# Performance work log

Hardware: AMD Instinct MI355X
Metric: run time of the kernel (lower is better)

The kernel has to match this reference:

```python
import jax, jax.numpy as jnp
import numpy as np

N = 131072   # num_nodes
E = 262144   # events in the batch
D = 128      # memory_dim
R = 128      # raw_msg_dim
T = 32       # time_dim


def setup_inputs() -> dict:
    key = jax.random.key(0)
    ks = jax.random.split(key, 16)
    s = 0.05
    return {
        "memory": jax.random.normal(ks[0], (N, D), jnp.float32) * s,
        "raw_msg": jax.random.normal(ks[1], (E, R), jnp.float32) * s,
        "time_w": jax.random.normal(ks[2], (T,), jnp.float32) * s,
        "time_b": jax.random.normal(ks[3], (T,), jnp.float32) * s,
        "W_msg_s": jax.random.normal(ks[4], (D, 2 * D + R + T), jnp.float32) * s,
        "b_msg_s": jax.random.normal(ks[5], (D,), jnp.float32) * s,
        "W_msg_d": jax.random.normal(ks[6], (D, 2 * D + R + T), jnp.float32) * s,
        "b_msg_d": jax.random.normal(ks[7], (D,), jnp.float32) * s,
        "W_ih": jax.random.normal(ks[8], (3 * D, D), jnp.float32) * s,
        "W_hh": jax.random.normal(ks[9], (3 * D, D), jnp.float32) * s,
        "b_ih": jax.random.normal(ks[10], (3 * D,), jnp.float32) * s,
        "b_hh": jax.random.normal(ks[11], (3 * D,), jnp.float32) * s,
        "src": jax.random.randint(ks[12], (E,), 0, N, jnp.int32),
        "dst": jax.random.randint(ks[13], (E,), 0, N, jnp.int32),
        "t": jax.random.randint(ks[14], (E,), 0, 100000, jnp.int32),
        "last_update": jax.random.randint(ks[15], (N,), 0, 50000, jnp.int32),
    }


def _time_enc(t_rel, time_w, time_b):
    # TimeEncoder: cos(Linear(t)) ; t_rel: [E] float -> [E, T]
    return jnp.cos(t_rel[:, None] * time_w[None, :] + time_b[None, :])


def _message(mem_a, mem_b, raw_msg, t_enc, W, b):
    # message MLP on concat(mem_src, mem_dst, raw_msg, t_enc)
    x = jnp.concatenate([mem_a, mem_b, raw_msg, t_enc], axis=-1)  # [E, 2D+R+T]
    return jax.nn.relu(x @ W.T + b)


def _forward(memory, raw_msg, time_w, time_b, W_msg_s, b_msg_s, W_msg_d, b_msg_d,
             W_ih, W_hh, b_ih, b_hh, src, dst, t, last_update):
    tf = t.astype(jnp.float32)
    lu = last_update.astype(jnp.float32)
    mem_s = memory[src]  # gather [E, D]
    mem_d = memory[dst]

    # source-side messages (stored under key src): t_rel = t - last_update[src]
    t_enc_s = _time_enc(tf - lu[src], time_w, time_b)
    msg_s = _message(mem_s, mem_d, raw_msg, t_enc_s, W_msg_s, b_msg_s)
    # dest-side messages (stored under key dst, src/dst swapped)
    t_enc_d = _time_enc(tf - lu[dst], time_w, time_b)
    msg_d = _message(mem_d, mem_s, raw_msg, t_enc_d, W_msg_d, b_msg_d)

    # scatter mean-aggregate messages onto their owner node
    seg = jnp.concatenate([src, dst], axis=0)          # [2E]
    vals = jnp.concatenate([msg_s, msg_d], axis=0)     # [2E, D]
    sums = jax.ops.segment_sum(vals, seg, num_segments=N)
    cnt = jax.ops.segment_sum(jnp.ones((2 * E,), jnp.float32), seg, num_segments=N)
    aggr = sums / jnp.maximum(cnt, 1.0)[:, None]       # [N, D]

    # GRUCell(aggr, memory)
    gi = aggr @ W_ih.T + b_ih
    gh = memory @ W_hh.T + b_hh
    i_r, i_z, i_n = jnp.split(gi, 3, axis=-1)
    h_r, h_z, h_n = jnp.split(gh, 3, axis=-1)
    r = jax.nn.sigmoid(i_r + h_r)
    z = jax.nn.sigmoid(i_z + h_z)
    n = jnp.tanh(i_n + r * h_n)
    new_memory = (1.0 - z) * n + z * memory

    # scatter-max timestamps (pyg scatter reduce='max' fills empty slots with 0)
    tt = jnp.concatenate([t, t], axis=0)
    seg_max = jax.ops.segment_max(tt, seg, num_segments=N)
    new_last_update = jnp.where(cnt > 0, seg_max, jnp.zeros((), jnp.int32))
    return new_memory, new_last_update


def reference(memory, raw_msg, time_w, time_b, W_msg_s, b_msg_s, W_msg_d, b_msg_d,
              W_ih, W_hh, b_ih, b_hh, src, dst, t, last_update):
    return _forward(memory, raw_msg, time_w, time_b, W_msg_s, b_msg_s, W_msg_d,
                    b_msg_d, W_ih, W_hh, b_ih, b_hh, src, dst, t, last_update)
```

## Files before the change

kernel.cpp:

```cpp
#include <hip/hip_runtime.h>
#include <cstdint>
#include <cstddef>

#define NN 131072
#define EE 262144
#define DD 128

typedef __attribute__((ext_vector_type(8))) short bf16x8;
typedef __attribute__((ext_vector_type(4))) float f32x4;

__device__ __forceinline__ unsigned short f2bf(float f) {
    unsigned int u = __builtin_bit_cast(unsigned int, f);
    u += 0x7FFFu + ((u >> 16) & 1u);
    return (unsigned short)(u >> 16);
}
__device__ __forceinline__ float bf2f(unsigned short s) {
    unsigned int u = ((unsigned int)s) << 16;
    return __builtin_bit_cast(float, u);
}
__device__ __forceinline__ float sigmoidf_(float x) { return 1.0f / (1.0f + __expf(-x)); }
__device__ __forceinline__ float tanhf_(float x) {
    float ax = fabsf(x);
    float e = __expf(-2.0f * ax);
    return copysignf((1.0f - e) / (1.0f + e), x);
}

__global__ void k_prep_wmsg(const float* __restrict__ Ws, const float* __restrict__ Wd,
                            const float* __restrict__ bs, const float* __restrict__ bd,
                            unsigned short* __restrict__ Wm, float* __restrict__ bm) {
    int n = blockIdx.x;
    int k = threadIdx.x;
    float v;
    if (n < 128) {
        v = (k < 416) ? Ws[n * 416 + k] : 0.0f;
    } else {
        int m = n - 128;
        if (k < 128)       v = Wd[m * 416 + 128 + k];
        else if (k < 256)  v = Wd[m * 416 + (k - 128)];
        else if (k < 384)  v = Wd[m * 416 + k];
        else if (k < 416)  v = 0.0f;
        else               v = Wd[m * 416 + 384 + (k - 416)];
    }
    Wm[n * 448 + k] = f2bf(v);
    if (blockIdx.x == 0 && k < 256) bm[k] = (k < 128) ? bs[k] : bd[k - 128];
}

__global__ void k_prep_wgru(const float* __restrict__ Wih, const float* __restrict__ Whh,
                            const float* __restrict__ bih, const float* __restrict__ bhh,
                            unsigned short* __restrict__ Wg, float* __restrict__ bg) {
    int j = blockIdx.x;
    int k = threadIdx.x;
    float v;
    if (j < 256)       v = (k < 128) ? Wih[j * 128 + k] : Whh[j * 128 + (k - 128)];
    else if (j < 384)  v = (k < 128) ? Wih[j * 128 + k] : 0.0f;
    else               v = (k < 128) ? 0.0f : Whh[(j - 128) * 128 + (k - 128)];
    Wg[j * 256 + k] = f2bf(v);
    if (j == 0) {
        for (int i = k; i < 512; i += 256) {
            float b = (i < 256) ? (bih[i] + bhh[i]) : ((i < 384) ? bih[i] : bhh[i - 128]);
            bg[i] = b;
        }
    }
}

__global__ void k_memconv(const float* __restrict__ in, unsigned short* __restrict__ outp) {
    int gid = blockIdx.x * 256 + threadIdx.x;
    const float4 v = ((const float4*)in)[gid];
    ushort4 o;
    o.x = f2bf(v.x); o.y = f2bf(v.y); o.z = f2bf(v.z); o.w = f2bf(v.w);
    *(ushort4*)(outp + (size_t)gid * 4) = o;
}

__global__ void k_trel(const int* __restrict__ t, const int* __restrict__ src,
                       const int* __restrict__ dst, const int* __restrict__ lu,
                       float* __restrict__ trel_s, float* __restrict__ trel_d) {
    int e = blockIdx.x * 256 + threadIdx.x;
    int tv = t[e];
    trel_s[e] = (float)(tv - lu[src[e]]);
    trel_d[e] = (float)(tv - lu[dst[e]]);
}

__global__ void k_cnt(const int* __restrict__ src, const int* __restrict__ dst,
                      const int* __restrict__ t, int* cnt, int* lu_tmp) {
    int e = blockIdx.x * 256 + threadIdx.x;
    int s = src[e], d = dst[e], tv = t[e];
    atomicAdd(&cnt[s], 1);
    atomicAdd(&cnt[d], 1);
    atomicMax(&lu_tmp[s], tv);
    atomicMax(&lu_tmp[d], tv);
}

__global__ void k_scan1(const int* __restrict__ cnt, int* __restrict__ bsum) {
    __shared__ int red[256];
    int tid = threadIdx.x;
    red[tid] = cnt[blockIdx.x * 256 + tid];
    __syncthreads();
    for (int s = 128; s > 0; s >>= 1) {
        if (tid < s) red[tid] += red[tid + s];
        __syncthreads();
    }
    if (tid == 0) bsum[blockIdx.x] = red[0];
}
__global__ void k_scan2(const int* __restrict__ bsum, int* __restrict__ boff) {
    __shared__ int sb[512];
    int tid = threadIdx.x;
    int v = bsum[tid];
    sb[tid] = v;
    __syncthreads();
    for (int d = 1; d < 512; d <<= 1) {
        int u = (tid >= d) ? sb[tid - d] : 0;
        __syncthreads();
        sb[tid] += u;
        __syncthreads();
    }
    boff[tid] = sb[tid] - v;
}
__global__ void k_scan3(const int* __restrict__ cnt, const int* __restrict__ boff,
                        int* __restrict__ off, int* __restrict__ cursor) {
    __shared__ int sb[256];
    int tid = threadIdx.x;
    int i = blockIdx.x * 256 + tid;
    int v = cnt[i];
    sb[tid] = v;
    __syncthreads();
    for (int d = 1; d < 256; d <<= 1) {
        int u = (tid >= d) ? sb[tid - d] : 0;
        __syncthreads();
        sb[tid] += u;
        __syncthreads();
    }
    int o = boff[blockIdx.x] + sb[tid] - v;
    off[i] = o;
    cursor[i] = o;
}
__global__ void k_fill(const int* __restrict__ src, const int* __restrict__ dst,
                       int* cursor, int* __restrict__ ids) {
    int e2 = blockIdx.x * 256 + threadIdx.x;
    int node = (e2 < EE) ? src[e2] : dst[e2 - EE];
    int pos = atomicAdd(&cursor[node], 1);
    ids[pos] = e2;
}

__launch_bounds__(256, 2)
__global__ void k_msg(const unsigned short* __restrict__ memb,
                      const float* __restrict__ raw,
                      const float* __restrict__ trel_s,
                      const float* __restrict__ trel_d,
                      const unsigned short* __restrict__ Wm,
                      const float* __restrict__ bm,
                      const int* __restrict__ src, const int* __restrict__ dst,
                      const float* __restrict__ tw, const float* __restrict__ tb,
                      unsigned short* __restrict__ msg) {
    __shared__ int s_idx[128], d_idx[128];
    __shared__ float s_tw[32], s_tb[32];
    __shared__ __align__(16) unsigned short As[128 * 40];
    __shared__ __align__(16) unsigned short Bs[256 * 40];

    const int tid = threadIdx.x;
    const int e0 = blockIdx.x * 128;
    if (tid < 128) s_idx[tid] = src[e0 + tid];
    else           d_idx[tid - 128] = dst[e0 + tid - 128];
    if (tid < 32)       s_tw[tid] = tw[tid];
    else if (tid < 64)  s_tb[tid - 32] = tb[tid - 32];
    __syncthreads();

    const int lane = tid & 63, w = tid >> 6;
    const int col0 = lane & 15, q = lane >> 4;

    f32x4 acc[8][4];
#pragma unroll
    for (int a = 0; a < 8; ++a)
#pragma unroll
        for (int b = 0; b < 4; ++b)
#pragma unroll
            for (int i = 0; i < 4; ++i) acc[a][b][i] = 0.0f;

    for (int c = 0; c < 14; ++c) {
#pragma unroll
        for (int i = 0; i < 4; ++i) {
            int lin = tid + 256 * i;
            int row = lin >> 2, seg = lin & 3;
            bf16x8 v = *(const bf16x8*)(Wm + (size_t)row * 448 + c * 32 + seg * 8);
            *(bf16x8*)&Bs[row * 40 + seg * 8] = v;
        }
        if (c < 8) {
#pragma unroll
            for (int i = 0; i < 2; ++i) {
                int lin = tid + 256 * i;
                int row = lin >> 2, seg = lin & 3;
                int node = (c < 4) ? s_idx[row] : d_idx[row];
                bf16x8 v = *(const bf16x8*)(memb + (size_t)node * 128 + (c & 3) * 32 + seg * 8);
                *(bf16x8*)&As[row * 40 + seg * 8] = v;
            }
        } else if (c < 12) {
#pragma unroll
            for (int i = 0; i < 4; ++i) {
                int lin = tid + 256 * i;
                int row = lin >> 3, seg = lin & 7;
                const float4 v = *(const float4*)(raw + (size_t)(e0 + row) * 128 + (c - 8) * 32 + seg * 4);
                unsigned short* p = &As[row * 40 + seg * 4];
                p[0] = f2bf(v.x); p[1] = f2bf(v.y); p[2] = f2bf(v.z); p[3] = f2bf(v.w);
            }
        } else {
            int row = tid >> 1, half = tid & 1;
            float tr = (c == 12) ? trel_s[e0 + row] : trel_d[e0 + row];
            unsigned short* p = &As[row * 40 + half * 16];
#pragma unroll
            for (int j2 = 0; j2 < 16; ++j2) {
                int jj = half * 16 + j2;
                p[j2] = f2bf(__cosf(tr * s_tw[jj] + s_tb[jj]));
            }
        }
        __syncthreads();

        bf16x8 afr[8], bfr[4];
#pragma unroll
        for (int mt = 0; mt < 8; ++mt)
            afr[mt] = *(const bf16x8*)&As[(mt * 16 + col0) * 40 + q * 8];
#pragma unroll
        for (int nl = 0; nl < 4; ++nl)
            bfr[nl] = *(const bf16x8*)&Bs[((w * 4 + nl) * 16 + col0) * 40 + q * 8];
#pragma unroll
        for (int mt = 0; mt < 8; ++mt)
#pragma unroll
            for (int nl = 0; nl < 4; ++nl)
                acc[mt][nl] = __builtin_amdgcn_mfma_f32_16x16x32_bf16(afr[mt], bfr[nl], acc[mt][nl], 0, 0, 0);
        __syncthreads();
    }

#pragma unroll
    for (int nl = 0; nl < 4; ++nl) {
        int j = (w * 4 + nl) * 16 + col0;
        float bv = bm[j];
        int feat = j & 127;
        size_t base = (j < 128) ? (size_t)0 : (size_t)EE * 128;
#pragma unroll
        for (int mt = 0; mt < 8; ++mt) {
#pragma unroll
            for (int r = 0; r < 4; ++r) {
                int ev = mt * 16 + q * 4 + r;
                float v = fmaxf(acc[mt][nl][r] + bv, 0.0f);
                msg[base + (size_t)(e0 + ev) * 128 + feat] = f2bf(v);
            }
        }
    }
}

__launch_bounds__(256, 2)
__global__ void k_gru(const unsigned short* __restrict__ msg,
                      const int* __restrict__ off, const int* __restrict__ cnt,
                      const int* __restrict__ ids,
                      const float* __restrict__ memory,
                      const unsigned short* __restrict__ Wg,
                      const float* __restrict__ bg,
                      float* __restrict__ out) {
    __shared__ __align__(16) unsigned short Xs[64 * 264];
    __shared__ __align__(16) unsigned short Bs[512 * 40];

    const int tid = threadIdx.x;
    const int n0 = blockIdx.x * 64;

    {
        int g = tid >> 2, sub = tid & 3;
        int node = n0 + g;
        int beg = off[node], cn = cnt[node];
        float a[32];
#pragma unroll
        for (int i = 0; i < 32; ++i) a[i] = 0.0f;
        for (int m = 0; m < cn; ++m) {
            int id = ids[beg + m];
            const bf16x8* p = (const bf16x8*)(msg + (size_t)id * 128 + sub * 32);
#pragma unroll
            for (int s = 0; s < 4; ++s) {
                bf16x8 v = p[s];
#pragma unroll
                for (int k = 0; k < 8; ++k)
                    a[s * 8 + k] += bf2f((unsigned short)v[k]);
            }
        }
        float inv = 1.0f / (float)(cn > 1 ? cn : 1);
        unsigned short* xp = &Xs[g * 264 + sub * 32];
#pragma unroll
        for (int i = 0; i < 32; ++i) xp[i] = f2bf(a[i] * inv);
        const float4* mp = (const float4*)(memory + (size_t)node * 128 + sub * 32);
        unsigned short* xq = &Xs[g * 264 + 128 + sub * 32];
#pragma unroll
        for (int s = 0; s < 8; ++s) {
            float4 v = mp[s];
            xq[s * 4 + 0] = f2bf(v.x); xq[s * 4 + 1] = f2bf(v.y);
            xq[s * 4 + 2] = f2bf(v.z); xq[s * 4 + 3] = f2bf(v.w);
        }
    }

    const int lane = tid & 63, w = tid >> 6;
    const int col0 = lane & 15, q = lane >> 4;

    f32x4 acc[4][4][2];
#pragma unroll
    for (int a = 0; a < 4; ++a)
#pragma unroll
        for (int g = 0; g < 4; ++g)
#pragma unroll
            for (int f = 0; f < 2; ++f)
#pragma unroll
                for (int i = 0; i < 4; ++i) acc[a][g][f][i] = 0.0f;

    for (int c = 0; c < 8; ++c) {
#pragma unroll
        for (int i = 0; i < 8; ++i) {
            int lin = tid + 256 * i;
            int row = lin >> 2, seg = lin & 3;
            bf16x8 v = *(const bf16x8*)(Wg + (size_t)row * 256 + c * 32 + seg * 8);
            *(bf16x8*)&Bs[row * 40 + seg * 8] = v;
        }
        __syncthreads();

        bf16x8 afr[4], bfr[4][2];
#pragma unroll
        for (int mt = 0; mt < 4; ++mt)
            afr[mt] = *(const bf16x8*)&Xs[(mt * 16 + col0) * 264 + c * 32 + q * 8];
#pragma unroll
        for (int g = 0; g < 4; ++g)
#pragma unroll
            for (int fh = 0; fh < 2; ++fh) {
                int nt = 8 * g + 2 * w + fh;
                bfr[g][fh] = *(const bf16x8*)&Bs[(nt * 16 + col0) * 40 + q * 8];
            }
#pragma unroll
        for (int mt = 0; mt < 4; ++mt)
#pragma unroll
            for (int g = 0; g < 4; ++g)
#pragma unroll
                for (int fh = 0; fh < 2; ++fh)
                    acc[mt][g][fh] = __builtin_amdgcn_mfma_f32_16x16x32_bf16(afr[mt], bfr[g][fh], acc[mt][g][fh], 0, 0, 0);
        __syncthreads();
    }

#pragma unroll
    for (int fh = 0; fh < 2; ++fh) {
        int feat = w * 32 + fh * 16 + col0;
        float b_r = bg[feat], b_z = bg[128 + feat], b_in = bg[256 + feat], b_hn = bg[384 + feat];
#pragma unroll
        for (int mt = 0; mt < 4; ++mt) {
#pragma unroll
            for (int r = 0; r < 4; ++r) {
                int node = n0 + mt * 16 + q * 4 + r;
                float rr = sigmoidf_(acc[mt][0][fh][r] + b_r);
                float zz = sigmoidf_(acc[mt][1][fh][r] + b_z);
                float nn = tanhf_((acc[mt][2][fh][r] + b_in) + rr * (acc[mt][3][fh][r] + b_hn));
                float h = memory[(size_t)node * 128 + feat];
                out[(size_t)node * 128 + feat] = (1.0f - zz) * nn + zz * h;
            }
        }
    }
}

__global__ void k_lu(const int* __restrict__ lu_tmp, float* __restrict__ outp) {
    int i = blockIdx.x * 256 + threadIdx.x;
    outp[i] = (float)lu_tmp[i];
}

extern "C" void kernel_launch(void* const* d_in, const int* in_sizes, int n_in,
                              void* d_out, int out_size, void* d_ws, size_t ws_size,
                              hipStream_t stream) {
    const float* memory = (const float*)d_in[0];
    const float* raw    = (const float*)d_in[1];
    const float* tw     = (const float*)d_in[2];
    const float* tb     = (const float*)d_in[3];
    const float* Wms    = (const float*)d_in[4];
    const float* bms    = (const float*)d_in[5];
    const float* Wmd    = (const float*)d_in[6];
    const float* bmd    = (const float*)d_in[7];
    const float* Wih    = (const float*)d_in[8];
    const float* Whh    = (const float*)d_in[9];
    const float* bih    = (const float*)d_in[10];
    const float* bhh    = (const float*)d_in[11];
    const int* src = (const int*)d_in[12];
    const int* dst = (const int*)d_in[13];
    const int* t   = (const int*)d_in[14];
    const int* lu  = (const int*)d_in[15];

    char* ws = (char*)d_ws;
    size_t off_b = 0;
    unsigned short* memb = (unsigned short*)(ws + off_b); off_b += (size_t)NN * 128 * 2;
    unsigned short* msg  = (unsigned short*)(ws + off_b); off_b += (size_t)2 * EE * 128 * 2;
    float* trel_s        = (float*)(ws + off_b);          off_b += (size_t)EE * 4;
    float* trel_d        = (float*)(ws + off_b);          off_b += (size_t)EE * 4;
    int* cnt             = (int*)(ws + off_b);            off_b += (size_t)NN * 4;
    int* off             = (int*)(ws + off_b);            off_b += (size_t)NN * 4;
    int* cursor          = (int*)(ws + off_b);            off_b += (size_t)NN * 4;
    int* lu_tmp          = (int*)(ws + off_b);            off_b += (size_t)NN * 4;
    int* ids             = (int*)(ws + off_b);            off_b += (size_t)2 * EE * 4;
    int* bsum            = (int*)(ws + off_b);            off_b += 512 * 4;
    int* boff            = (int*)(ws + off_b);            off_b += 512 * 4;
    unsigned short* Wm   = (unsigned short*)(ws + off_b); off_b += 256 * 448 * 2;
    float* bm            = (float*)(ws + off_b);          off_b += 256 * 4;
    unsigned short* Wg   = (unsigned short*)(ws + off_b); off_b += 512 * 256 * 2;
    float* bg            = (float*)(ws + off_b);          off_b += 512 * 4;

    float* out = (float*)d_out;

    hipMemsetAsync(cnt, 0, (size_t)NN * 4, stream);
    hipMemsetAsync(lu_tmp, 0, (size_t)NN * 4, stream);

    k_prep_wmsg<<<256, 448, 0, stream>>>(Wms, Wmd, bms, bmd, Wm, bm);
    k_prep_wgru<<<512, 256, 0, stream>>>(Wih, Whh, bih, bhh, Wg, bg);
    k_memconv<<<(NN * 128 / 4) / 256, 256, 0, stream>>>(memory, memb);
    k_trel<<<EE / 256, 256, 0, stream>>>(t, src, dst, lu, trel_s, trel_d);
    k_cnt<<<EE / 256, 256, 0, stream>>>(src, dst, t, cnt, lu_tmp);
    k_scan1<<<512, 256, 0, stream>>>(cnt, bsum);
    k_scan2<<<1, 512, 0, stream>>>(bsum, boff);
    k_scan3<<<512, 256, 0, stream>>>(cnt, boff, off, cursor);
    k_fill<<<2 * EE / 256, 256, 0, stream>>>(src, dst, cursor, ids);
    k_msg<<<EE / 128, 256, 0, stream>>>(memb, raw, trel_s, trel_d, Wm, bm, src, dst, tw, tb, msg);
    k_gru<<<NN / 64, 256, 0, stream>>>(msg, off, cnt, ids, memory, Wg, bg, out);
    k_lu<<<NN / 256, 256, 0, stream>>>(lu_tmp, out + (size_t)NN * 128);
}
```

Before: 623.9 us.

## Prepack weights as MFMA fragments, write messages in CSR order, double-buffer A tiles

Weights are pre-packed into per-lane MFMA fragment order so both GEMM kernels read B operands straight from global memory instead of staging them through shared memory. The message kernel double-buffers the A tile and scatters each message row to its sorted CSR slot. That lets the GRU kernel read contiguous message rows without an indirection through ids. The trel and count kernels are fused, and the GRU kernel uses 32-node blocks with higher occupancy, no per-chunk syncs, and vectorized bf16 packing. The cost is scattered msg writes and repeated global weight loads per block, which rely on caching.

```diff
diff --git a/kernel.cpp b/kernel.cpp
--- a/kernel.cpp
+++ b/kernel.cpp
@@ -4,7 +4,6 @@
 
 #define NN 131072
 #define EE 262144
-#define DD 128
 
 typedef __attribute__((ext_vector_type(8))) short bf16x8;
 typedef __attribute__((ext_vector_type(4))) float f32x4;
@@ -24,43 +23,62 @@
     float e = __expf(-2.0f * ax);
     return copysignf((1.0f - e) / (1.0f + e), x);
 }
-
-__global__ void k_prep_wmsg(const float* __restrict__ Ws, const float* __restrict__ Wd,
-                            const float* __restrict__ bs, const float* __restrict__ bd,
-                            unsigned short* __restrict__ Wm, float* __restrict__ bm) {
-    int n = blockIdx.x;
-    int k = threadIdx.x;
-    float v;
+__device__ __forceinline__ bf16x8 pack8(const float* f) {
+    bf16x8 o;
+#pragma unroll
+    for (int i = 0; i < 8; ++i) o[i] = (short)f2bf(f[i]);
+    return o;
+}
+
+__device__ __forceinline__ float wmsg_val(int n, int k, const float* Ws, const float* Wd) {
     if (n < 128) {
-        v = (k < 416) ? Ws[n * 416 + k] : 0.0f;
+        return (k < 416) ? Ws[n * 416 + k] : 0.0f;
     } else {
         int m = n - 128;
-        if (k < 128)       v = Wd[m * 416 + 128 + k];
-        else if (k < 256)  v = Wd[m * 416 + (k - 128)];
-        else if (k < 384)  v = Wd[m * 416 + k];
-        else if (k < 416)  v = 0.0f;
-        else               v = Wd[m * 416 + 384 + (k - 416)];
-    }
-    Wm[n * 448 + k] = f2bf(v);
-    if (blockIdx.x == 0 && k < 256) bm[k] = (k < 128) ? bs[k] : bd[k - 128];
-}
-
-__global__ void k_prep_wgru(const float* __restrict__ Wih, const float* __restrict__ Whh,
-                            const float* __restrict__ bih, const float* __restrict__ bhh,
-                            unsigned short* __restrict__ Wg, float* __restrict__ bg) {
-    int j = blockIdx.x;
-    int k = threadIdx.x;
-    float v;
-    if (j < 256)       v = (k < 128) ? Wih[j * 128 + k] : Whh[j * 128 + (k - 128)];
-    else if (j < 384)  v = (k < 128) ? Wih[j * 128 + k] : 0.0f;
-    else               v = (k < 128) ? 0.0f : Whh[(j - 128) * 128 + (k - 128)];
-    Wg[j * 256 + k] = f2bf(v);
-    if (j == 0) {
-        for (int i = k; i < 512; i += 256) {
-            float b = (i < 256) ? (bih[i] + bhh[i]) : ((i < 384) ? bih[i] : bhh[i - 128]);
-            bg[i] = b;
-        }
-    }
+        if (k < 128)       return Wd[m * 416 + 128 + k];
+        else if (k < 256)  return Wd[m * 416 + (k - 128)];
+        else if (k < 384)  return Wd[m * 416 + k];
+        else if (k < 416)  return 0.0f;
+        else               return Wd[m * 416 + 384 + (k - 416)];
+    }
+}
+__device__ __forceinline__ float wgru_val(int j, int k, const float* Wih, const float* Whh) {
+    if (j < 256)      return (k < 128) ? Wih[j * 128 + k] : Whh[j * 128 + (k - 128)];
+    else if (j < 384) return (k < 128) ? Wih[j * 128 + k] : 0.0f;
+    else              return (k < 128) ? 0.0f : Whh[(j - 128) * 128 + (k - 128)];
+}
+
+__global__ void k_prep_msgfrag(const float* __restrict__ Ws, const float* __restrict__ Wd,
+                               const float* __restrict__ bs, const float* __restrict__ bd,
+                               unsigned short* __restrict__ Wmf, float* __restrict__ bm) {
+    int b = blockIdx.x;
+    int c = b >> 4, nt = b & 15;
+    int lane = threadIdx.x;
+    int col0 = lane & 15, q = lane >> 4;
+    int n = nt * 16 + col0;
+    float f[8];
+#pragma unroll
+    for (int j = 0; j < 8; ++j) f[j] = wmsg_val(n, c * 32 + q * 8 + j, Ws, Wd);
+    ((bf16x8*)Wmf)[(size_t)b * 64 + lane] = pack8(f);
+    if (b == 0)
+        for (int i = lane; i < 256; i += 64) bm[i] = (i < 128) ? bs[i] : bd[i - 128];
+}
+
+__global__ void k_prep_grufrag(const float* __restrict__ Wih, const float* __restrict__ Whh,
+                               const float* __restrict__ bih, const float* __restrict__ bhh,
+                               unsigned short* __restrict__ Wgf, float* __restrict__ bg) {
+    int b = blockIdx.x;
+    int c = b >> 5, nt = b & 31;
+    int lane = threadIdx.x;
+    int col0 = lane & 15, q = lane >> 4;
+    int j0 = nt * 16 + col0;
+    float f[8];
+#pragma unroll
+    for (int j = 0; j < 8; ++j) f[j] = wgru_val(j0, c * 32 + q * 8 + j, Wih, Whh);
+    ((bf16x8*)Wgf)[(size_t)b * 64 + lane] = pack8(f);
+    if (b == 0)
+        for (int i = lane; i < 512; i += 64)
+            bg[i] = (i < 256) ? (bih[i] + bhh[i]) : ((i < 384) ? bih[i] : bhh[i - 128]);
 }
 
 __global__ void k_memconv(const float* __restrict__ in, unsigned short* __restrict__ outp) {
@@ -71,19 +89,14 @@
     *(ushort4*)(outp + (size_t)gid * 4) = o;
 }
 
-__global__ void k_trel(const int* __restrict__ t, const int* __restrict__ src,
-                       const int* __restrict__ dst, const int* __restrict__ lu,
-                       float* __restrict__ trel_s, float* __restrict__ trel_d) {
-    int e = blockIdx.x * 256 + threadIdx.x;
-    int tv = t[e];
-    trel_s[e] = (float)(tv - lu[src[e]]);
-    trel_d[e] = (float)(tv - lu[dst[e]]);
-}
-
-__global__ void k_cnt(const int* __restrict__ src, const int* __restrict__ dst,
-                      const int* __restrict__ t, int* cnt, int* lu_tmp) {
+__global__ void k_pre(const int* __restrict__ t, const int* __restrict__ src,
+                      const int* __restrict__ dst, const int* __restrict__ lu,
+                      float* __restrict__ trel_s, float* __restrict__ trel_d,
+                      int* cnt, int* lu_tmp) {
     int e = blockIdx.x * 256 + threadIdx.x;
     int s = src[e], d = dst[e], tv = t[e];
+    trel_s[e] = (float)(tv - lu[s]);
+    trel_d[e] = (float)(tv - lu[d]);
     atomicAdd(&cnt[s], 1);
     atomicAdd(&cnt[d], 1);
     atomicMax(&lu_tmp[s], tv);
@@ -134,11 +147,10 @@
     cursor[i] = o;
 }
 __global__ void k_fill(const int* __restrict__ src, const int* __restrict__ dst,
-                       int* cursor, int* __restrict__ ids) {
+                       int* cursor, int* __restrict__ pos2) {
     int e2 = blockIdx.x * 256 + threadIdx.x;
     int node = (e2 < EE) ? src[e2] : dst[e2 - EE];
-    int pos = atomicAdd(&cursor[node], 1);
-    ids[pos] = e2;
+    pos2[e2] = atomicAdd(&cursor[node], 1);
 }
 
 __launch_bounds__(256, 2)
@@ -146,20 +158,20 @@
                       const float* __restrict__ raw,
                       const float* __restrict__ trel_s,
                       const float* __restrict__ trel_d,
-                      const unsigned short* __restrict__ Wm,
+                      const unsigned short* __restrict__ Wmf,
                       const float* __restrict__ bm,
                       const int* __restrict__ src, const int* __restrict__ dst,
+                      const int* __restrict__ pos2,
                       const float* __restrict__ tw, const float* __restrict__ tb,
                       unsigned short* __restrict__ msg) {
-    __shared__ int s_idx[128], d_idx[128];
+    __shared__ int s_idx[128], d_idx[128], s_pos[128], d_pos[128];
     __shared__ float s_tw[32], s_tb[32];
-    __shared__ __align__(16) unsigned short As[128 * 40];
-    __shared__ __align__(16) unsigned short Bs[256 * 40];
+    __shared__ __align__(16) unsigned short As[2][128 * 40];
 
     const int tid = threadIdx.x;
     const int e0 = blockIdx.x * 128;
-    if (tid < 128) s_idx[tid] = src[e0 + tid];
-    else           d_idx[tid - 128] = dst[e0 + tid - 128];
+    if (tid < 128) { s_idx[tid] = src[e0 + tid]; s_pos[tid] = pos2[e0 + tid]; }
+    else { d_idx[tid - 128] = dst[e0 + tid - 128]; d_pos[tid - 128] = pos2[EE + e0 + tid - 128]; }
     if (tid < 32)       s_tw[tid] = tw[tid];
     else if (tid < 64)  s_tb[tid - 32] = tb[tid - 32];
     __syncthreads();
@@ -167,59 +179,64 @@
     const int lane = tid & 63, w = tid >> 6;
     const int col0 = lane & 15, q = lane >> 4;
 
-    f32x4 acc[8][4];
-#pragma unroll
-    for (int a = 0; a < 8; ++a)
-#pragma unroll
-        for (int b = 0; b < 4; ++b)
-#pragma unroll
-            for (int i = 0; i < 4; ++i) acc[a][b][i] = 0.0f;
-
-    for (int c = 0; c < 14; ++c) {
-#pragma unroll
-        for (int i = 0; i < 4; ++i) {
-            int lin = tid + 256 * i;
-            int row = lin >> 2, seg = lin & 3;
-            bf16x8 v = *(const bf16x8*)(Wm + (size_t)row * 448 + c * 32 + seg * 8);
-            *(bf16x8*)&Bs[row * 40 + seg * 8] = v;
-        }
-        if (c < 8) {
+    auto stage = [&](int cc) {
+        unsigned short* A = As[cc & 1];
+        if (cc < 8) {
 #pragma unroll
             for (int i = 0; i < 2; ++i) {
                 int lin = tid + 256 * i;
                 int row = lin >> 2, seg = lin & 3;
-                int node = (c < 4) ? s_idx[row] : d_idx[row];
-                bf16x8 v = *(const bf16x8*)(memb + (size_t)node * 128 + (c & 3) * 32 + seg * 8);
-                *(bf16x8*)&As[row * 40 + seg * 8] = v;
-            }
-        } else if (c < 12) {
+                int node = (cc < 4) ? s_idx[row] : d_idx[row];
+                bf16x8 v = *(const bf16x8*)(memb + (size_t)node * 128 + (cc & 3) * 32 + seg * 8);
+                *(bf16x8*)&A[row * 40 + seg * 8] = v;
+            }
+        } else if (cc < 12) {
 #pragma unroll
             for (int i = 0; i < 4; ++i) {
                 int lin = tid + 256 * i;
                 int row = lin >> 3, seg = lin & 7;
-                const float4 v = *(const float4*)(raw + (size_t)(e0 + row) * 128 + (c - 8) * 32 + seg * 4);
-                unsigned short* p = &As[row * 40 + seg * 4];
-                p[0] = f2bf(v.x); p[1] = f2bf(v.y); p[2] = f2bf(v.z); p[3] = f2bf(v.w);
+                const float4 v = *(const float4*)(raw + (size_t)(e0 + row) * 128 + (cc - 8) * 32 + seg * 4);
+                ushort4 o;
+                o.x = f2bf(v.x); o.y = f2bf(v.y); o.z = f2bf(v.z); o.w = f2bf(v.w);
+                *(ushort4*)&A[row * 40 + seg * 4] = o;
             }
         } else {
             int row = tid >> 1, half = tid & 1;
-            float tr = (c == 12) ? trel_s[e0 + row] : trel_d[e0 + row];
-            unsigned short* p = &As[row * 40 + half * 16];
+            float tr = (cc == 12) ? trel_s[e0 + row] : trel_d[e0 + row];
+            float f[16];
 #pragma unroll
             for (int j2 = 0; j2 < 16; ++j2) {
                 int jj = half * 16 + j2;
-                p[j2] = f2bf(__cosf(tr * s_tw[jj] + s_tb[jj]));
-            }
+                f[j2] = __cosf(tr * s_tw[jj] + s_tb[jj]);
+            }
+            *(bf16x8*)&A[row * 40 + half * 16] = pack8(&f[0]);
+            *(bf16x8*)&A[row * 40 + half * 16 + 8] = pack8(&f[8]);
         }
-        __syncthreads();
-
-        bf16x8 afr[8], bfr[4];
+    };
+
+    f32x4 acc[8][4];
+#pragma unroll
+    for (int a = 0; a < 8; ++a)
+#pragma unroll
+        for (int b = 0; b < 4; ++b)
+#pragma unroll
+            for (int i = 0; i < 4; ++i) acc[a][b][i] = 0.0f;
+
+    stage(0);
+    __syncthreads();
+
+    for (int c = 0; c < 14; ++c) {
+        bf16x8 bfr[4];
+        const bf16x8* Wc = (const bf16x8*)Wmf + (size_t)c * 16 * 64;
+#pragma unroll
+        for (int nl = 0; nl < 4; ++nl)
+            bfr[nl] = Wc[(w * 4 + nl) * 64 + lane];
+        const unsigned short* A = As[c & 1];
+        bf16x8 afr[8];
 #pragma unroll
         for (int mt = 0; mt < 8; ++mt)
-            afr[mt] = *(const bf16x8*)&As[(mt * 16 + col0) * 40 + q * 8];
-#pragma unroll
-        for (int nl = 0; nl < 4; ++nl)
-            bfr[nl] = *(const bf16x8*)&Bs[((w * 4 + nl) * 16 + col0) * 40 + q * 8];
+            afr[mt] = *(const bf16x8*)&A[(mt * 16 + col0) * 40 + q * 8];
+        if (c < 13) stage(c + 1);
 #pragma unroll
         for (int mt = 0; mt < 8; ++mt)
 #pragma unroll
@@ -233,71 +250,71 @@
         int j = (w * 4 + nl) * 16 + col0;
         float bv = bm[j];
         int feat = j & 127;
-        size_t base = (j < 128) ? (size_t)0 : (size_t)EE * 128;
+        bool is_s = (j < 128);
 #pragma unroll
         for (int mt = 0; mt < 8; ++mt) {
 #pragma unroll
             for (int r = 0; r < 4; ++r) {
                 int ev = mt * 16 + q * 4 + r;
                 float v = fmaxf(acc[mt][nl][r] + bv, 0.0f);
-                msg[base + (size_t)(e0 + ev) * 128 + feat] = f2bf(v);
+                int pos = is_s ? s_pos[ev] : d_pos[ev];
+                msg[(size_t)pos * 128 + feat] = f2bf(v);
             }
         }
     }
 }
 
-__launch_bounds__(256, 2)
+__launch_bounds__(256, 3)
 __global__ void k_gru(const unsigned short* __restrict__ msg,
                       const int* __restrict__ off, const int* __restrict__ cnt,
-                      const int* __restrict__ ids,
                       const float* __restrict__ memory,
-                      const unsigned short* __restrict__ Wg,
+                      const unsigned short* __restrict__ Wgf,
                       const float* __restrict__ bg,
                       float* __restrict__ out) {
-    __shared__ __align__(16) unsigned short Xs[64 * 264];
-    __shared__ __align__(16) unsigned short Bs[512 * 40];
+    __shared__ __align__(16) unsigned short Xs[32 * 264];
 
     const int tid = threadIdx.x;
-    const int n0 = blockIdx.x * 64;
+    const int n0 = blockIdx.x * 32;
 
     {
-        int g = tid >> 2, sub = tid & 3;
+        int g = tid >> 3, sub = tid & 7;
         int node = n0 + g;
         int beg = off[node], cn = cnt[node];
-        float a[32];
-#pragma unroll
-        for (int i = 0; i < 32; ++i) a[i] = 0.0f;
+        float a[16];
+#pragma unroll
+        for (int i = 0; i < 16; ++i) a[i] = 0.0f;
         for (int m = 0; m < cn; ++m) {
-            int id = ids[beg + m];
-            const bf16x8* p = (const bf16x8*)(msg + (size_t)id * 128 + sub * 32);
-#pragma unroll
-            for (int s = 0; s < 4; ++s) {
-                bf16x8 v = p[s];
-#pragma unroll
-                for (int k = 0; k < 8; ++k)
-                    a[s * 8 + k] += bf2f((unsigned short)v[k]);
+            const bf16x8* p = (const bf16x8*)(msg + (size_t)(beg + m) * 128 + sub * 16);
+            bf16x8 v0 = p[0], v1 = p[1];
+#pragma unroll
+            for (int k = 0; k < 8; ++k) {
+                a[k]     += bf2f((unsigned short)v0[k]);
+                a[8 + k] += bf2f((unsigned short)v1[k]);
             }
         }
         float inv = 1.0f / (float)(cn > 1 ? cn : 1);
-        unsigned short* xp = &Xs[g * 264 + sub * 32];
-#pragma unroll
-        for (int i = 0; i < 32; ++i) xp[i] = f2bf(a[i] * inv);
-        const float4* mp = (const float4*)(memory + (size_t)node * 128 + sub * 32);
-        unsigned short* xq = &Xs[g * 264 + 128 + sub * 32];
-#pragma unroll
-        for (int s = 0; s < 8; ++s) {
+#pragma unroll
+        for (int i = 0; i < 16; ++i) a[i] *= inv;
+        *(bf16x8*)&Xs[g * 264 + sub * 16] = pack8(&a[0]);
+        *(bf16x8*)&Xs[g * 264 + sub * 16 + 8] = pack8(&a[8]);
+        float f[16];
+        const float4* mp = (const float4*)(memory + (size_t)node * 128 + sub * 16);
+#pragma unroll
+        for (int s = 0; s < 4; ++s) {
             float4 v = mp[s];
-            xq[s * 4 + 0] = f2bf(v.x); xq[s * 4 + 1] = f2bf(v.y);
-            xq[s * 4 + 2] = f2bf(v.z); xq[s * 4 + 3] = f2bf(v.w);
+            f[s * 4 + 0] = v.x; f[s * 4 + 1] = v.y; f[s * 4 + 2] = v.z; f[s * 4 + 3] = v.w;
         }
-    }
+        *(bf16x8*)&Xs[g * 264 + 128 + sub * 16] = pack8(&f[0]);
+        *(bf16x8*)&Xs[g * 264 + 128 + sub * 16 + 8] = pack8(&f[8]);
+    }
+    __syncthreads();
 
     const int lane = tid & 63, w = tid >> 6;
     const int col0 = lane & 15, q = lane >> 4;
 
-    f32x4 acc[4][4][2];
-#pragma unroll
-    for (int a = 0; a < 4; ++a)
+    f32x4 acc[2][4][2];
+#pragma unroll
+    for (int a = 0; a < 2; ++a)
 #pragma unroll
         for (int g = 0; g < 4; ++g)
 #pragma unroll
@@ -305,35 +322,26 @@
 #pragma unroll
                 for (int i = 0; i < 4; ++i) acc[a][g][f][i] = 0.0f;
 
+#pragma unroll
     for (int c = 0; c < 8; ++c) {
-#pragma unroll
-        for (int i = 0; i < 8; ++i) {
-            int lin = tid + 256 * i;
-            int row = lin >> 2, seg = lin & 3;
-            bf16x8 v = *(const bf16x8*)(Wg + (size_t)row * 256 + c * 32 + seg * 8);
-            *(bf16x8*)&Bs[row * 40 + seg * 8] = v;
-        }
-        __syncthreads();
-
-        bf16x8 afr[4], bfr[4][2];
-#pragma unroll
-        for (int mt = 0; mt < 4; ++mt)
+        bf16x8 bfr[4][2];
+        const bf16x8* Wc = (const bf16x8*)Wgf + (size_t)c * 32 * 64;
+#pragma unroll
+        for (int g = 0; g < 4; ++g)
+#pragma unroll
+            for (int fh = 0; fh < 2; ++fh)
+                bfr[g][fh] = Wc[(8 * g + 2 * w + fh) * 64 + lane];
+        bf16x8 afr[2];
+#pragma unroll
+        for (int mt = 0; mt < 2; ++mt)
             afr[mt] = *(const bf16x8*)&Xs[(mt * 16 + col0) * 264 + c * 32 + q * 8];
 #pragma unroll
-        for (int g = 0; g < 4; ++g)
-#pragma unroll
-            for (int fh = 0; fh < 2; ++fh) {
-                int nt = 8 * g + 2 * w + fh;
-                bfr[g][fh] = *(const bf16x8*)&Bs[(nt * 16 + col0) * 40 + q * 8];
-            }
-#pragma unroll
-        for (int mt = 0; mt < 4; ++mt)
+        for (int mt = 0; mt < 2; ++mt)
 #pragma unroll
             for (int g = 0; g < 4; ++g)
 #pragma unroll
                 for (int fh = 0; fh < 2; ++fh)
                     acc[mt][g][fh] = __builtin_amdgcn_mfma_f32_16x16x32_bf16(afr[mt], bfr[g][fh], acc[mt][g][fh], 0, 0, 0);
-        __syncthreads();
     }
 
 #pragma unroll
@@ -341,7 +349,7 @@
         int feat = w * 32 + fh * 16 + col0;
         float b_r = bg[feat], b_z = bg[128 + feat], b_in = bg[256 + feat], b_hn = bg[384 + feat];
 #pragma unroll
-        for (int mt = 0; mt < 4; ++mt) {
+        for (int mt = 0; mt < 2; ++mt) {
 #pragma unroll
             for (int r = 0; r < 4; ++r) {
                 int node = n0 + mt * 16 + q * 4 + r;
@@ -381,38 +389,37 @@
     const int* lu  = (const int*)d_in[15];
 
     char* ws = (char*)d_ws;
-    size_t off_b = 0;
-    unsigned short* memb = (unsigned short*)(ws + off_b); off_b += (size_t)NN * 128 * 2;
-    unsigned short* msg  = (unsigned short*)(ws + off_b); off_b += (size_t)2 * EE * 128 * 2;
-    float* trel_s        = (float*)(ws + off_b);          off_b += (size_t)EE * 4;
-    float* trel_d        = (float*)(ws + off_b);          off_b += (size_t)EE * 4;
-    int* cnt             = (int*)(ws + off_b);            off_b += (size_t)NN * 4;
-    int* off             = (int*)(ws + off_b);            off_b += (size_t)NN * 4;
-    int* cursor          = (int*)(ws + off_b);            off_b += (size_t)NN * 4;
-    int* lu_tmp          = (int*)(ws + off_b);            off_b += (size_t)NN * 4;
-    int* ids             = (int*)(ws + off_b);            off_b += (size_t)2 * EE * 4;
-    int* bsum            = (int*)(ws + off_b);            off_b += 512 * 4;
-    int* boff            = (int*)(ws + off_b);            off_b += 512 * 4;
-    unsigned short* Wm   = (unsigned short*)(ws + off_b); off_b += 256 * 448 * 2;
-    float* bm            = (float*)(ws + off_b);          off_b += 256 * 4;
-    unsigned short* Wg   = (unsigned short*)(ws + off_b); off_b += 512 * 256 * 2;
-    float* bg            = (float*)(ws + off_b);          off_b += 512 * 4;
+    size_t ob = 0;
+    unsigned short* memb = (unsigned short*)(ws + ob); ob += (size_t)NN * 128 * 2;
+    unsigned short* msg  = (unsigned short*)(ws + ob); ob += (size_t)2 * EE * 128 * 2;
+    float* trel_s        = (float*)(ws + ob);          ob += (size_t)EE * 4;
+    float* trel_d        = (float*)(ws + ob);          ob += (size_t)EE * 4;
+    int* cnt             = (int*)(ws + ob);            ob += (size_t)NN * 4;
+    int* off             = (int*)(ws + ob);            ob += (size_t)NN * 4;
+    int* cursor          = (int*)(ws + ob);            ob += (size_t)NN * 4;
+    int* lu_tmp          = (int*)(ws + ob);            ob += (size_t)NN * 4;
+    int* pos2            = (int*)(ws + ob);            ob += (size_t)2 * EE * 4;
+    int* bsum            = (int*)(ws + ob);            ob += 512 * 4;
+    int* boff            = (int*)(ws + ob);            ob += 512 * 4;
+    unsigned short* Wmf  = (unsigned short*)(ws + ob); ob += (size_t)14 * 16 * 64 * 8 * 2;
+    float* bm            = (float*)(ws + ob);          ob += 256 * 4;
+    unsigned short* Wgf  = (unsigned short*)(ws + ob); ob += (size_t)8 * 32 * 64 * 8 * 2;
+    float* bg            = (float*)(ws + ob);          ob += 512 * 4;
 
     float* out = (float*)d_out;
 
     hipMemsetAsync(cnt, 0, (size_t)NN * 4, stream);
     hipMemsetAsync(lu_tmp, 0, (size_t)NN * 4, stream);
 
-    k_prep_wmsg<<<256, 448, 0, stream>>>(Wms, Wmd, bms, bmd, Wm, bm);
-    k_prep_wgru<<<512, 256, 0, stream>>>(Wih, Whh, bih, bhh, Wg, bg);
+    k_prep_msgfrag<<<14 * 16, 64, 0, stream>>>(Wms, Wmd, bms, bmd, Wmf, bm);
+    k_prep_grufrag<<<8 * 32, 64, 0, stream>>>(Wih, Whh, bih, bhh, Wgf, bg);
     k_memconv<<<(NN * 128 / 4) / 256, 256, 0, stream>>>(memory, memb);
-    k_trel<<<EE / 256, 256, 0, stream>>>(t, src, dst, lu, trel_s, trel_d);
-    k_cnt<<<EE / 256, 256, 0, stream>>>(src, dst, t, cnt, lu_tmp);
+    k_pre<<<EE / 256, 256, 0, stream>>>(t, src, dst, lu, trel_s, trel_d, cnt, lu_tmp);
     k_scan1<<<512, 256, 0, stream>>>(cnt, bsum);
     k_scan2<<<1, 512, 0, stream>>>(bsum, boff);
     k_scan3<<<512, 256, 0, stream>>>(cnt, boff, off, cursor);
-    k_fill<<<2 * EE / 256, 256, 0, stream>>>(src, dst, cursor, ids);
-    k_msg<<<EE / 128, 256, 0, stream>>>(memb, raw, trel_s, trel_d, Wm, bm, src, dst, tw, tb, msg);
-    k_gru<<<NN / 64, 256, 0, stream>>>(msg, off, cnt, ids, memory, Wg, bg, out);
+    k_fill<<<2 * EE / 256, 256, 0, stream>>>(src, dst, cursor, pos2);
+    k_msg<<<EE / 128, 256, 0, stream>>>(memb, raw, trel_s, trel_d, Wmf, bm, src, dst, pos2, tw, tb, msg);
+    k_gru<<<NN / 32, 256, 0, stream>>>(msg, off, cnt, memory, Wgf, bg, out);
     k_lu<<<NN / 256, 256, 0, stream>>>(lu_tmp, out + (size_t)NN * 128);
 }
```

Result: faster. 579.0 us (-7.2%).
